# Kernel tuning notes

Hardware: AMD Instinct MI355X
Metric: run time of the kernel (lower is better)

The kernel has to match this reference:

```python
import jax, jax.numpy as jnp
import numpy as np

S, B, E, H = 2048, 2, 1024, 16
HD = E // H

def setup_inputs() -> dict:
    key = jax.random.key(0)
    ks = jax.random.split(key, 5)
    return {
        "query": jax.random.normal(ks[0], (S, B, E), dtype=jnp.float32),
        "key": jax.random.normal(ks[1], (S, B, E), dtype=jnp.float32),
        "value": jax.random.normal(ks[2], (S, B, E), dtype=jnp.float32),
        "in_proj_weight": jax.random.normal(ks[3], (3 * E, E), dtype=jnp.float32) * (E ** -0.5),
        "out_weight": jax.random.normal(ks[4], (E, E), dtype=jnp.float32) * (E ** -0.5),
    }

def reference(query, key, value, in_proj_weight, out_weight):
    # query: [S, B, E]; key/value are ignored by the original self-attn module.
    seq_len, bsz, embed_dim = query.shape
    head_dim = embed_dim // H
    scaling = head_dim ** -0.5
    # qkv projection: [S, B, 3E]; the torch view splits 3E as (H, 3, head_dim)
    qkv = jnp.einsum('sbe,fe->sbf', query, in_proj_weight)
    qkv = qkv.reshape(seq_len, bsz, H, 3, head_dim)
    q = qkv[..., 0, :]  # [S, B, H, hd]
    k = qkv[..., 1, :]
    v = qkv[..., 2, :]
    # scores: [B, H, S, S] (materialized, as in the unfused original)
    scores = jnp.einsum('sbhd,tbhd->bhst', q, k) * scaling
    probs = jax.nn.softmax(scores, axis=-1)
    attn = jnp.einsum('bhst,tbhd->sbhd', probs, v)
    attn = attn.reshape(seq_len, bsz, embed_dim)
    out = jnp.einsum('sbe,fe->sbf', attn, out_weight)
    return out
```

## Files before the change

kernel.cpp:

```cpp
#include <hip/hip_runtime.h>

typedef __attribute__((ext_vector_type(8))) short bf16x8;
typedef __attribute__((ext_vector_type(4))) float f32x4;
typedef __attribute__((ext_vector_type(8))) unsigned short u16x8;
typedef __attribute__((ext_vector_type(4))) unsigned short u16x4;

#define S_LEN 2048
#define BATCH 2
#define EMB 1024
#define NH 16
#define HDIM 64
#define M_ROWS (S_LEN * BATCH)
#define N_QKV (3 * EMB)

typedef const __attribute__((address_space(1))) unsigned int* gptr_t;
typedef __attribute__((address_space(3))) unsigned int* lptr_t;

__device__ __forceinline__ unsigned short f2b(float f) {
  union { float f; unsigned u; } v; v.f = f;
  unsigned r = v.u + 0x7fff + ((v.u >> 16) & 1);
  return (unsigned short)(r >> 16);
}

__global__ __launch_bounds__(256) void cvt_f32_bf16(const float* __restrict__ in,
                                                    unsigned short* __restrict__ out,
                                                    int n4) {
  int i = blockIdx.x * 256 + threadIdx.x;
  if (i >= n4) return;
  float4 a = reinterpret_cast<const float4*>(in)[i];
  u16x4 o;
  o[0] = f2b(a.x); o[1] = f2b(a.y); o[2] = f2b(a.z); o[3] = f2b(a.w);
  reinterpret_cast<u16x4*>(out)[i] = o;
}

template <int OUT_BF16>
__global__ __launch_bounds__(256) void gemm_bt(const unsigned short* __restrict__ A,
                                               const unsigned short* __restrict__ Bm,
                                               void* __restrict__ Cv,
                                               int Md, int Nd, int Kd) {
  __shared__ unsigned short As[128][32];
  __shared__ unsigned short Bs[128][32];
  int t = threadIdx.x;
  int bm = blockIdx.y, bn = blockIdx.x;
  int wid = t >> 6, lane = t & 63;
  int wr = wid >> 1, wc = wid & 1;
  int fr = lane & 15, fq = lane >> 4;
  int lrow = lane >> 2;
  int lcol = (lane & 3) * 8;

  f32x4 acc[4][4];
#pragma unroll
  for (int i = 0; i < 4; ++i)
#pragma unroll
    for (int j = 0; j < 4; ++j) acc[i][j] = (f32x4){0.f, 0.f, 0.f, 0.f};

  int nkt = Kd >> 5;
  for (int kt = 0; kt < nkt; ++kt) {
    const unsigned short* ga = A + (size_t)(bm * 128 + wid * 32 + lrow) * Kd + kt * 32 + lcol;
    const unsigned short* gb = Bm + (size_t)(bn * 128 + wid * 32 + lrow) * Kd + kt * 32 + lcol;
#pragma unroll
    for (int j = 0; j < 2; ++j) {
      __builtin_amdgcn_global_load_lds((gptr_t)(ga + (size_t)j * 16 * Kd),
                                       (lptr_t)&As[wid * 32 + j * 16][0], 16, 0, 0);
      __builtin_amdgcn_global_load_lds((gptr_t)(gb + (size_t)j * 16 * Kd),
                                       (lptr_t)&Bs[wid * 32 + j * 16][0], 16, 0, 0);
    }
    __syncthreads();

    bf16x8 af[4], bfv[4];
#pragma unroll
    for (int mt = 0; mt < 4; ++mt)
      af[mt] = *reinterpret_cast<const bf16x8*>(&As[wr * 64 + mt * 16 + fr][fq * 8]);
#pragma unroll
    for (int nt = 0; nt < 4; ++nt)
      bfv[nt] = *reinterpret_cast<const bf16x8*>(&Bs[wc * 64 + nt * 16 + fr][fq * 8]);
#pragma unroll
    for (int mt = 0; mt < 4; ++mt)
#pragma unroll
      for (int nt = 0; nt < 4; ++nt)
        acc[mt][nt] = __builtin_amdgcn_mfma_f32_16x16x32_bf16(af[mt], bfv[nt], acc[mt][nt], 0, 0, 0);
    __syncthreads();
  }

#pragma unroll
  for (int mt = 0; mt < 4; ++mt)
#pragma unroll
    for (int nt = 0; nt < 4; ++nt)
#pragma unroll
      for (int r = 0; r < 4; ++r) {
        int row = bm * 128 + wr * 64 + mt * 16 + fq * 4 + r;
        int col = bn * 128 + wc * 64 + nt * 16 + fr;
        float val = acc[mt][nt][r];
        if (OUT_BF16)
          reinterpret_cast<unsigned short*>(Cv)[(size_t)row * Nd + col] = f2b(val);
        else
          reinterpret_cast<float*>(Cv)[(size_t)row * Nd + col] = val;
      }
}

__global__ __launch_bounds__(256) void vtrans(const unsigned short* __restrict__ qkv,
                                              unsigned short* __restrict__ vt) {
  __shared__ unsigned short Ts[64][72];
  int t = threadIdx.x;
  int kb = blockIdx.x;
  int bh = blockIdx.y;
  int b = bh >> 4, h = bh & 15;
  int k0 = kb * 64;
#pragma unroll
  for (int i = 0; i < 2; ++i) {
    int c = t + i * 256;
    int r = c >> 3, q = c & 7;
    int chunk = q ^ ((r >> 3) & 7);
    *reinterpret_cast<u16x8*>(&Ts[r][chunk * 8]) =
        *reinterpret_cast<const u16x8*>(
            qkv + ((size_t)(k0 + r) * BATCH + b) * N_QKV + h * 192 + 128 + q * 8);
  }
  __syncthreads();
#pragma unroll
  for (int i = 0; i < 2; ++i) {
    int c = t + i * 256;
    int d = c >> 3, q = c & 7;
    u16x8 o;
#pragma unroll
    for (int j = 0; j < 8; ++j) {
      int k = q * 8 + j;
      int chunk = (d >> 3) ^ q;
      o[j] = Ts[k][chunk * 8 + (d & 7)];
    }
    *reinterpret_cast<u16x8*>(&vt[((size_t)bh * 64 + d) * S_LEN + k0 + q * 8]) = o;
  }
}

__global__ __launch_bounds__(256) void attn_kernel(const unsigned short* __restrict__ qkv,
                                                   const unsigned short* __restrict__ vt,
                                                   unsigned short* __restrict__ att) {
  __shared__ unsigned short Ks[64][72];
  __shared__ unsigned short VtS[64][72];
  __shared__ unsigned short Ps[4][16][72];
  int t = threadIdx.x;
  int wid = t >> 6, lane = t & 63;
  int fr = lane & 15, fq = lane >> 4;
  int bh = blockIdx.y;
  int b = bh >> 4;
  int h = bh & 15;
  int q0 = blockIdx.x * 64;

  int qi = q0 + wid * 16 + fr;
  const unsigned short* qrow = qkv + ((size_t)qi * BATCH + b) * N_QKV + h * 192;
  bf16x8 qf[2];
  qf[0] = *reinterpret_cast<const bf16x8*>(qrow + fq * 8);
  qf[1] = *reinterpret_cast<const bf16x8*>(qrow + 32 + fq * 8);

  f32x4 o[4];
#pragma unroll
  for (int dt = 0; dt < 4; ++dt) o[dt] = (f32x4){0.f, 0.f, 0.f, 0.f};
  float m_run[4], l_run[4];
#pragma unroll
  for (int r = 0; r < 4; ++r) { m_run[r] = -1e30f; l_run[r] = 0.f; }

  for (int kt = 0; kt < S_LEN / 64; ++kt) {
#pragma unroll
    for (int i = 0; i < 2; ++i) {
      int c = t + i * 256;
      int row = c >> 3, c8 = (c & 7) * 8;
      *reinterpret_cast<u16x8*>(&Ks[row][c8]) = *reinterpret_cast<const u16x8*>(
          qkv + ((size_t)(kt * 64 + row) * BATCH + b) * N_QKV + h * 192 + 64 + c8);
      *reinterpret_cast<u16x8*>(&VtS[row][c8]) = *reinterpret_cast<const u16x8*>(
          vt + ((size_t)bh * 64 + row) * S_LEN + kt * 64 + c8);
    }
    __syncthreads();

    f32x4 sf[4];
#pragma unroll
    for (int nt = 0; nt < 4; ++nt) {
      bf16x8 bk0 = *reinterpret_cast<const bf16x8*>(&Ks[nt * 16 + fr][fq * 8]);
      bf16x8 bk1 = *reinterpret_cast<const bf16x8*>(&Ks[nt * 16 + fr][32 + fq * 8]);
      f32x4 s = (f32x4){0.f, 0.f, 0.f, 0.f};
      s = __builtin_amdgcn_mfma_f32_16x16x32_bf16(qf[0], bk0, s, 0, 0, 0);
      s = __builtin_amdgcn_mfma_f32_16x16x32_bf16(qf[1], bk1, s, 0, 0, 0);
      sf[nt] = s;
    }
#pragma unroll
    for (int nt = 0; nt < 4; ++nt) sf[nt] *= 0.125f;

    float p[4][4];
#pragma unroll
    for (int r = 0; r < 4; ++r) {
      float mx = fmaxf(fmaxf(sf[0][r], sf[1][r]), fmaxf(sf[2][r], sf[3][r]));
#pragma unroll
      for (int m = 1; m < 16; m <<= 1) mx = fmaxf(mx, __shfl_xor(mx, m));
      float mnew = fmaxf(m_run[r], mx);
      float alpha = __expf(m_run[r] - mnew);
      m_run[r] = mnew;
      float rs = 0.f;
#pragma unroll
      for (int nt = 0; nt < 4; ++nt) {
        float pv = __expf(sf[nt][r] - mnew);
        p[nt][r] = pv;
        rs += pv;
      }
#pragma unroll
      for (int m = 1; m < 16; m <<= 1) rs += __shfl_xor(rs, m);
      l_run[r] = l_run[r] * alpha + rs;
#pragma unroll
      for (int dt = 0; dt < 4; ++dt) o[dt][r] *= alpha;
    }

#pragma unroll
    for (int nt = 0; nt < 4; ++nt)
#pragma unroll
      for (int r = 0; r < 4; ++r)
        Ps[wid][fq * 4 + r][nt * 16 + fr] = f2b(p[nt][r]);

#pragma unroll
    for (int kc = 0; kc < 2; ++kc) {
      bf16x8 pa = *reinterpret_cast<const bf16x8*>(&Ps[wid][fr][kc * 32 + fq * 8]);
#pragma unroll
      for (int dt = 0; dt < 4; ++dt) {
        bf16x8 vb = *reinterpret_cast<const bf16x8*>(&VtS[dt * 16 + fr][kc * 32 + fq * 8]);
        o[dt] = __builtin_amdgcn_mfma_f32_16x16x32_bf16(pa, vb, o[dt], 0, 0, 0);
      }
    }
    __syncthreads();
  }

#pragma unroll
  for (int dt = 0; dt < 4; ++dt)
#pragma unroll
    for (int r = 0; r < 4; ++r) {
      int q = q0 + wid * 16 + fq * 4 + r;
      int d = dt * 16 + fr;
      float val = o[dt][r] / l_run[r];
      att[((size_t)q * BATCH + b) * EMB + h * 64 + d] = f2b(val);
    }
}

extern "C" void kernel_launch(void* const* d_in, const int* in_sizes, int n_in,
                              void* d_out, int out_size, void* d_ws, size_t ws_size,
                              hipStream_t stream) {
  const float* q_in  = (const float*)d_in[0];
  const float* w_in  = (const float*)d_in[3];
  const float* w_out = (const float*)d_in[4];
  float* out = (float*)d_out;

  unsigned short* ws  = (unsigned short*)d_ws;
  unsigned short* Xb  = ws;
  unsigned short* Wb  = Xb + (size_t)M_ROWS * EMB;
  unsigned short* Ob  = Wb + (size_t)N_QKV * EMB;
  unsigned short* QKV = Ob + (size_t)EMB * EMB;
  unsigned short* ATT = QKV + (size_t)M_ROWS * N_QKV;
  unsigned short* Vt  = Xb;

  cvt_f32_bf16<<<(M_ROWS * EMB / 4 + 255) / 256, 256, 0, stream>>>(q_in, Xb, M_ROWS * EMB / 4);
  cvt_f32_bf16<<<(N_QKV * EMB / 4 + 255) / 256, 256, 0, stream>>>(w_in, Wb, N_QKV * EMB / 4);
  cvt_f32_bf16<<<(EMB * EMB / 4 + 255) / 256, 256, 0, stream>>>(w_out, Ob, EMB * EMB / 4);

  gemm_bt<1><<<dim3(N_QKV / 128, M_ROWS / 128), 256, 0, stream>>>(Xb, Wb, QKV, M_ROWS, N_QKV, EMB);
  vtrans<<<dim3(S_LEN / 64, BATCH * NH), 256, 0, stream>>>(QKV, Vt);
  attn_kernel<<<dim3(S_LEN / 64, BATCH * NH), 256, 0, stream>>>(QKV, Vt, ATT);
  gemm_bt<0><<<dim3(EMB / 128, M_ROWS / 128), 256, 0, stream>>>(ATT, Ob, out, M_ROWS, EMB, EMB);
}
```

Measured before the change: 290.9 us.

## Double-buffer K/V tiles in attention via register prefetch, fold scale into Q

The attention kernel now keeps two LDS buffers for K and V^T. The next tile is loaded into registers during the current tile's MFMA and softmax work and written to the other buffer afterwards, so one barrier per iteration remains and global load latency can hide behind compute. The 1/8 softmax scale is folded into the Q fragments once, and P is rounded to bf16 with a cheaper conversion. The costs are extra LDS and registers, which may reduce occupancy, plus slightly different rounding for Q and P.

```diff
diff --git a/kernel.cpp b/kernel.cpp
--- a/kernel.cpp
+++ b/kernel.cpp
@@ -20,6 +20,14 @@
   union { float f; unsigned u; } v; v.f = f;
   unsigned r = v.u + 0x7fff + ((v.u >> 16) & 1);
   return (unsigned short)(r >> 16);
+}
+__device__ __forceinline__ unsigned short f2b_fast(float f) {
+  union { float f; unsigned u; } v; v.f = f;
+  return (unsigned short)((v.u + 0x8000u) >> 16);
+}
+__device__ __forceinline__ float b2f(unsigned short s) {
+  union { float f; unsigned u; } v; v.u = ((unsigned)s) << 16;
+  return v.f;
 }
 
 __global__ __launch_bounds__(256) void cvt_f32_bf16(const float* __restrict__ in,
@@ -134,8 +142,8 @@
 __global__ __launch_bounds__(256) void attn_kernel(const unsigned short* __restrict__ qkv,
                                                    const unsigned short* __restrict__ vt,
                                                    unsigned short* __restrict__ att) {
-  __shared__ unsigned short Ks[64][72];
-  __shared__ unsigned short VtS[64][72];
+  __shared__ unsigned short Ks[2][64][72];
+  __shared__ unsigned short VtS[2][64][72];
   __shared__ unsigned short Ps[4][16][72];
   int t = threadIdx.x;
   int wid = t >> 6, lane = t & 63;
@@ -145,11 +153,18 @@
   int h = bh & 15;
   int q0 = blockIdx.x * 64;
 
+  int srow = t >> 3, sc8 = (t & 7) * 8;
+
   int qi = q0 + wid * 16 + fr;
   const unsigned short* qrow = qkv + ((size_t)qi * BATCH + b) * N_QKV + h * 192;
   bf16x8 qf[2];
   qf[0] = *reinterpret_cast<const bf16x8*>(qrow + fq * 8);
   qf[1] = *reinterpret_cast<const bf16x8*>(qrow + 32 + fq * 8);
+#pragma unroll
+  for (int c = 0; c < 2; ++c)
+#pragma unroll
+    for (int j = 0; j < 8; ++j)
+      qf[c][j] = (short)f2b_fast(0.125f * b2f((unsigned short)qf[c][j]));
 
   f32x4 o[4];
 #pragma unroll
@@ -158,30 +173,41 @@
 #pragma unroll
   for (int r = 0; r < 4; ++r) { m_run[r] = -1e30f; l_run[r] = 0.f; }
 
+#pragma unroll
+  for (int i = 0; i < 2; ++i) {
+    int row = srow + i * 32;
+    *reinterpret_cast<u16x8*>(&Ks[0][row][sc8]) = *reinterpret_cast<const u16x8*>(
+        qkv + ((size_t)row * BATCH + b) * N_QKV + h * 192 + 64 + sc8);
+    *reinterpret_cast<u16x8*>(&VtS[0][row][sc8]) = *reinterpret_cast<const u16x8*>(
+        vt + ((size_t)bh * 64 + row) * S_LEN + sc8);
+  }
+  __syncthreads();
+
   for (int kt = 0; kt < S_LEN / 64; ++kt) {
-#pragma unroll
-    for (int i = 0; i < 2; ++i) {
-      int c = t + i * 256;
-      int row = c >> 3, c8 = (c & 7) * 8;
-      *reinterpret_cast<u16x8*>(&Ks[row][c8]) = *reinterpret_cast<const u16x8*>(
-          qkv + ((size_t)(kt * 64 + row) * BATCH + b) * N_QKV + h * 192 + 64 + c8);
-      *reinterpret_cast<u16x8*>(&VtS[row][c8]) = *reinterpret_cast<const u16x8*>(
-          vt + ((size_t)bh * 64 + row) * S_LEN + kt * 64 + c8);
-    }
-    __syncthreads();
+    int cur = kt & 1, nxt = cur ^ 1;
+
+    u16x8 kreg[2], vreg[2];
+    if (kt + 1 < S_LEN / 64) {
+#pragma unroll
+      for (int i = 0; i < 2; ++i) {
+        int row = srow + i * 32;
+        kreg[i] = *reinterpret_cast<const u16x8*>(
+            qkv + ((size_t)((kt + 1) * 64 + row) * BATCH + b) * N_QKV + h * 192 + 64 + sc8);
+        vreg[i] = *reinterpret_cast<const u16x8*>(
+            vt + ((size_t)bh * 64 + row) * S_LEN + (kt + 1) * 64 + sc8);
+      }
+    }
 
     f32x4 sf[4];
 #pragma unroll
     for (int nt = 0; nt < 4; ++nt) {
-      bf16x8 bk0 = *reinterpret_cast<const bf16x8*>(&Ks[nt * 16 + fr][fq * 8]);
-      bf16x8 bk1 = *reinterpret_cast<const bf16x8*>(&Ks[nt * 16 + fr][32 + fq * 8]);
+      bf16x8 bk0 = *reinterpret_cast<const bf16x8*>(&Ks[cur][nt * 16 + fr][fq * 8]);
+      bf16x8 bk1 = *reinterpret_cast<const bf16x8*>(&Ks[cur][nt * 16 + fr][32 + fq * 8]);
       f32x4 s = (f32x4){0.f, 0.f, 0.f, 0.f};
       s = __builtin_amdgcn_mfma_f32_16x16x32_bf16(qf[0], bk0, s, 0, 0, 0);
       s = __builtin_amdgcn_mfma_f32_16x16x32_bf16(qf[1], bk1, s, 0, 0, 0);
       sf[nt] = s;
     }
-#pragma unroll
-    for (int nt = 0; nt < 4; ++nt) sf[nt] *= 0.125f;
 
     float p[4][4];
 #pragma unroll
@@ -210,15 +236,24 @@
     for (int nt = 0; nt < 4; ++nt)
 #pragma unroll
       for (int r = 0; r < 4; ++r)
-        Ps[wid][fq * 4 + r][nt * 16 + fr] = f2b(p[nt][r]);
+        Ps[wid][fq * 4 + r][nt * 16 + fr] = f2b_fast(p[nt][r]);
 
 #pragma unroll
     for (int kc = 0; kc < 2; ++kc) {
       bf16x8 pa = *reinterpret_cast<const bf16x8*>(&Ps[wid][fr][kc * 32 + fq * 8]);
 #pragma unroll
       for (int dt = 0; dt < 4; ++dt) {
-        bf16x8 vb = *reinterpret_cast<const bf16x8*>(&VtS[dt * 16 + fr][kc * 32 + fq * 8]);
+        bf16x8 vb = *reinterpret_cast<const bf16x8*>(&VtS[cur][dt * 16 + fr][kc * 32 + fq * 8]);
         o[dt] = __builtin_amdgcn_mfma_f32_16x16x32_bf16(pa, vb, o[dt], 0, 0, 0);
+      }
+    }
+
+    if (kt + 1 < S_LEN / 64) {
+#pragma unroll
+      for (int i = 0; i < 2; ++i) {
+        int row = srow + i * 32;
+        *reinterpret_cast<u16x8*>(&Ks[nxt][row][sc8]) = kreg[i];
+        *reinterpret_cast<u16x8*>(&VtS[nxt][row][sc8]) = vreg[i];
       }
     }
     __syncthreads();
```

Result: no change. 294.9 us (+1.4%).
